# Optimization experiments

Measured on AMD Instinct MI355X. Metric: run time of the kernel, lower is better.

Reference implementation:

```python
import jax, jax.numpy as jnp
import numpy as np
from jax import lax

B = 32  # CS block size


def _conv(x, w, stride=1, pad=0):
    return lax.conv_general_dilated(
        x, w, window_strides=(stride, stride),
        padding=[(pad, pad), (pad, pad)],
        dimension_numbers=("NCHW", "OIHW", "NCHW"))


def _prelu(x, a):
    return jnp.where(x >= 0, x, a * x)


def _reshape_concat(x):
    # x: [N, B*B, h, w]; channel c = j*B + i maps to block pixel (i, j)
    # (tmp.view(B,B).permute(1,0) in the torch code). Blocks tile rows by
    # dim2 (h) and cols by dim3 (w). Vectorized depth-to-space + transpose.
    N, C, h, w = x.shape
    x5 = x.reshape(N, B, B, h, w)            # dims: (N, j, i, h, w)
    x5 = jnp.transpose(x5, (0, 3, 2, 4, 1))  # (N, h, i, w, j)
    return x5.reshape(N, 1, h * B, w * B)


def setup_inputs() -> dict:
    key = jax.random.key(0)
    ks = jax.random.split(key, 6)
    N, H, W = 16, 256, 256
    csnb = int(0.25 * B * B)  # 256
    inp = {
        "x": jax.random.normal(ks[0], (N, 1, H, W), jnp.float32),
        "W_cs": jax.random.normal(ks[1], (csnb, 1, B, B), jnp.float32) * 0.03,
        "W_init": jax.random.normal(ks[2], (B * B, csnb, 1, 1), jnp.float32) * 0.06,
        "W_first": jax.random.normal(ks[3], (64, 1, 3, 3), jnp.float32) * 0.3,
        "W_blk": jax.random.normal(ks[4], (64, 64, 3, 3), jnp.float32) * 0.04,
        "W_last": jax.random.normal(ks[5], (1, 64, 3, 3), jnp.float32) * 0.04,
        "a_main": jnp.full((1,), 0.1, jnp.float32),
        "a_blk": jnp.full((1,), 0.1, jnp.float32),
    }
    return inp


def reference(x, W_cs, W_init, W_first, W_blk, W_last, a_main, a_blk):
    # CS sampling: [N,1,H,W] -> [N,csnb,H/B,W/B]
    outcsy = _conv(x, W_cs, stride=B, pad=0)
    # initial reconstruction: 1x1 conv to B*B channels
    out = _conv(outcsy, W_init, stride=1, pad=0)
    out_initrec = _reshape_concat(out)          # [N,1,H,W]
    out = _prelu(_conv(out_initrec, W_first, pad=1), a_main)
    # same SORTRes_block (shared weights) applied 4 times
    for _ in range(4):
        o1 = _conv(out, W_blk, pad=1)
        o2 = _prelu(o1, a_blk)
        o3 = _conv(o2, W_blk, pad=1)
        out = _prelu(out + o3, a_blk)
    out = _conv(out + out_initrec, W_last, pad=1)
    return (out, outcsy, out_initrec)
```

## Files before the change

kernel.cpp:

```cpp
#include <hip/hip_runtime.h>
#include <hip/hip_bf16.h>
#include <initializer_list>


#define HW 65536
#define IMG 4194304

typedef __attribute__((ext_vector_type(8))) short short8;
typedef __attribute__((ext_vector_type(4))) float f32x4;

__device__ __forceinline__ float bf2f(unsigned short u) {
    union { unsigned u; float f; } v; v.u = ((unsigned)u) << 16; return v.f;
}
__device__ __forceinline__ unsigned short f2bf(float f) {
    union { float f; unsigned u; } v; v.f = f;
    unsigned r = v.u + 0x7FFF + ((v.u >> 16) & 1);
    return (unsigned short)(r >> 16);
}

__global__ void k_wcsT(const float* __restrict__ Wcs, float* __restrict__ WT)
{
    int e = blockIdx.x * 256 + threadIdx.x;
    int k = e >> 8, c = e & 255;
    WT[(long)k * 256 + c] = Wcs[(long)c * 1024 + k];
}

__global__ void k_winitT(const float* __restrict__ Wi, float* __restrict__ WT)
{
    int e = blockIdx.x * 256 + threadIdx.x;
    int ci = e >> 10, cc = e & 1023;
    WT[e] = Wi[(long)cc * 256 + ci];
}

__global__ __launch_bounds__(256) void k_cs2(const float* __restrict__ x,
        const float* __restrict__ WT, float* __restrict__ outcsy)
{
    __shared__ float xs[2][1024];
    const int b = blockIdx.x;
    const int tid = threadIdx.x;
#pragma unroll
    for (int t = 0; t < 2; ++t) {
        int p = b * 2 + t;
        int wb = p & 7, hb = (p >> 3) & 7, n = p >> 6;
#pragma unroll
        for (int i = 0; i < 4; ++i) {
            int k = tid + 256 * i;
            int ii = k >> 5, jj = k & 31;
            xs[t][k] = x[(long)n * HW + (hb * 32 + ii) * 256 + wb * 32 + jj];
        }
    }
    __syncthreads();
    float a0 = 0.f, a1 = 0.f;
    for (int k = 0; k < 1024; k += 8) {
#pragma unroll
        for (int u = 0; u < 8; ++u) {
            float wv = WT[(long)(k + u) * 256 + tid];
            a0 += wv * xs[0][k + u];
            a1 += wv * xs[1][k + u];
        }
    }
#pragma unroll
    for (int t = 0; t < 2; ++t) {
        int p = b * 2 + t;
        int wb = p & 7, hb = (p >> 3) & 7, n = p >> 6;
        float a = t ? a1 : a0;
        outcsy[(long)n * 16384 + tid * 64 + hb * 8 + wb] = a;
    }
}

__global__ __launch_bounds__(256) void k_init2(const float* __restrict__ outcsy,
        const float* __restrict__ WT, float* __restrict__ initrec)
{
    __shared__ float ys[2][256];
    __shared__ float ov[2][1024];
    const int b = blockIdx.x;
    const int np = b & 7, s = b >> 3;
    const int wb = s & 7, hb = s >> 3;
    const int tid = threadIdx.x;
#pragma unroll
    for (int i = 0; i < 2; ++i) {
        int idx = tid + 256 * i;
        int t = idx >> 8, c = idx & 255;
        ys[t][c] = outcsy[(long)(np * 2 + t) * 16384 + c * 64 + s];
    }
    __syncthreads();
#pragma unroll
    for (int q4 = 0; q4 < 4; ++q4) {
        int cc = q4 * 256 + tid;
        float a0 = 0.f, a1 = 0.f;
        for (int ci = 0; ci < 256; ci += 8) {
#pragma unroll
            for (int u = 0; u < 8; ++u) {
                float wv = WT[(long)(ci + u) * 1024 + cc];
                a0 += wv * ys[0][ci + u];
                a1 += wv * ys[1][ci + u];
            }
        }
        int i = cc & 31, j = cc >> 5;
        ov[0][i * 32 + j] = a0;
        ov[1][i * 32 + j] = a1;
    }
    __syncthreads();
#pragma unroll
    for (int t = 0; t < 2; ++t) {
        int n = np * 2 + t;
#pragma unroll
        for (int i2 = 0; i2 < 4; ++i2) {
            int p = i2 * 256 + tid;
            int i = p >> 5, j = p & 31;
            initrec[(long)n * HW + (hb * 32 + i) * 256 + wb * 32 + j] = ov[t][p];
        }
    }
}

__global__ __launch_bounds__(256) void k_first(const float* __restrict__ initrec,
        const float* __restrict__ Wf, unsigned short* __restrict__ A,
        const float* __restrict__ alpha_p)
{
    const int bid = blockIdx.x;
    const int tx = bid & 15, ty = (bid >> 4) & 15, n = bid >> 8;
    const int tid = threadIdx.x;
    const int x = (tx << 4) + (tid & 15), y = (ty << 4) + (tid >> 4);
    const float* ip = initrec + (long)n * HW;

    float in[9];
#pragma unroll
    for (int ky = 0; ky < 3; ++ky)
#pragma unroll
        for (int kx = 0; kx < 3; ++kx) {
            int iy = y + ky - 1, ix = x + kx - 1;
            in[ky * 3 + kx] = ((unsigned)iy < 256u && (unsigned)ix < 256u)
                                  ? ip[iy * 256 + ix] : 0.f;
        }

    const float alpha = alpha_p[0];
    unsigned short* op = &A[(((long)n * 256 + y) * 256 + x) * 64];
#pragma unroll
    for (int c8 = 0; c8 < 8; ++c8) {
        short8 ov;
#pragma unroll
        for (int j = 0; j < 8; ++j) {
            const float* wp = &Wf[(c8 * 8 + j) * 9];
            float a = 0.f;
#pragma unroll
            for (int t = 0; t < 9; ++t) a += wp[t] * in[t];
            a = a >= 0.f ? a : alpha * a;
            ov[j] = (short)f2bf(a);
        }
        *(short8*)&op[c8 * 8] = ov;
    }
}

__global__ void k_wprep(const float* __restrict__ Wb, unsigned short* __restrict__ Wp)
{
    int e = blockIdx.x * 256 + threadIdx.x;
    int cc = e / 18432, r = e % 18432;
    int tap = r / 2048, r2 = r % 2048;
    int nt = (r2 >> 9) & 3, l = (r2 >> 3) & 63, j = r2 & 7;
    int co = nt * 16 + (l & 15);
    int ci = cc * 32 + (l >> 4) * 8 + j;
    Wp[e] = f2bf(Wb[co * 576 + ci * 9 + tap]);
}

__global__ __launch_bounds__(256, 2) void k_res(const unsigned short* __restrict__ src,
        unsigned short* __restrict__ dst, const unsigned short* __restrict__ Wp,
        const float* __restrict__ alpha_p)
{
    __shared__ short smem[30400];

    const int tid = threadIdx.x;
    const int bid = blockIdx.x;
    const int tx = bid & 15, ty = (bid >> 4) & 15, n = bid >> 8;
    const int x0 = tx * 16, y0 = ty * 16;
    const int w = tid >> 6, lane = tid & 63;
    const int q = lane >> 4, mm = lane & 15;
    const float alpha = alpha_p[0];
    const unsigned short* sb = src + (long)n * IMG;

    int pb1[6];
#pragma unroll
    for (int i = 0; i < 6; ++i) {
        int p = (w + 4 * i) * 16 + mm;
        p = p < 323 ? p : 323;
        pb1[i] = p + 2 * (p / 18);
    }

#pragma unroll
    for (int i = 0; i < 13; ++i) {
        int idx = tid + 256 * i;
        if (idx < 3200) {
            int pix = idx >> 3, part = idx & 7;
            int row = pix / 20, col = pix - row * 20;
            int gy = y0 + row - 2, gx = x0 + col - 2;
            short8 v = {0, 0, 0, 0, 0, 0, 0, 0};
            if ((unsigned)gy < 256u && (unsigned)gx < 256u)
                v = *(const short8*)&sb[((long)gy * 256 + gx) * 64 + part * 8];
            *(short8*)&smem[pix * 76 + part * 8] = v;
        }
    }

    short8 bcur[4], bnxt[4];
#pragma unroll
    for (int nt = 0; nt < 4; ++nt)
        bcur[nt] = *(const short8*)&Wp[(size_t)(nt * 512 + lane * 8)];

    const f32x4 zz = {0.f, 0.f, 0.f, 0.f};
    f32x4 acc1[6][4];
#pragma unroll
    for (int i = 0; i < 6; ++i)
#pragma unroll
        for (int nt = 0; nt < 4; ++nt) acc1[i][nt] = zz;

    __syncthreads();

#pragma unroll
    for (int s = 0; s < 18; ++s) {
        const int cc = s / 9, tap = s % 9;
        int un = s + 1; un = un < 18 ? un : 0;
#pragma unroll
        for (int nt = 0; nt < 4; ++nt)
            bnxt[nt] = *(const short8*)&Wp[(size_t)(un / 9) * 18432 +
                       (size_t)(((un % 9) * 4 + nt) * 512 + lane * 8)];
        const int ky = tap / 3, kx = tap % 3;
        const int toff = (ky * 20 + kx) * 76 + cc * 32 + q * 8;
#pragma unroll
        for (int i = 0; i < 5; ++i) {
            short8 af = *(const short8*)&smem[pb1[i] * 76 + toff];
#pragma unroll
            for (int nt = 0; nt < 4; ++nt)
                acc1[i][nt] = __builtin_amdgcn_mfma_f32_16x16x32_bf16(
                    af, bcur[nt], acc1[i][nt], 0, 0, 0);
        }
        if (w == 0) {
            short8 af = *(const short8*)&smem[pb1[5] * 76 + toff];
#pragma unroll
            for (int nt = 0; nt < 4; ++nt)
                acc1[5][nt] = __builtin_amdgcn_mfma_f32_16x16x32_bf16(
                    af, bcur[nt], acc1[5][nt], 0, 0, 0);
        }
#pragma unroll
        for (int nt = 0; nt < 4; ++nt) bcur[nt] = bnxt[nt];
    }
    __syncthreads();

#pragma unroll
    for (int i = 0; i < 6; ++i) {
        int t = w + 4 * i;
        if (t < 21) {
#pragma unroll
            for (int r = 0; r < 4; ++r) {
                int p = t * 16 + q * 4 + r;
                p = p < 323 ? p : 323;
                int rho = p / 18, gam = p - 18 * rho;
                bool valid = (unsigned)(y0 - 1 + rho) < 256u &&
                             (unsigned)(x0 - 1 + gam) < 256u;
#pragma unroll
                for (int nt = 0; nt < 4; ++nt) {
                    float v = acc1[i][nt][r];
                    v = v >= 0.f ? v : alpha * v;
                    smem[p * 76 + nt * 16 + mm] = valid ? (short)f2bf(v) : (short)0;
                }
            }
        }
    }
    __syncthreads();

    f32x4 acc2[4][4];
#pragma unroll
    for (int mt = 0; mt < 4; ++mt)
#pragma unroll
        for (int nt = 0; nt < 4; ++nt) acc2[mt][nt] = zz;

#pragma unroll
    for (int s = 0; s < 18; ++s) {
        const int cc = s / 9, tap = s % 9;
        int un = s + 1; un = un < 18 ? un : 17;
#pragma unroll
        for (int nt = 0; nt < 4; ++nt)
            bnxt[nt] = *(const short8*)&Wp[(size_t)(un / 9) * 18432 +
                       (size_t)(((un % 9) * 4 + nt) * 512 + lane * 8)];
        const int ky = tap / 3, kx = tap % 3;
#pragma unroll
        for (int mt = 0; mt < 4; ++mt) {
            int pix = (4 * w + mt + ky) * 18 + mm + kx;
            short8 af = *(const short8*)&smem[pix * 76 + cc * 32 + q * 8];
#pragma unroll
            for (int nt = 0; nt < 4; ++nt)
                acc2[mt][nt] = __builtin_amdgcn_mfma_f32_16x16x32_bf16(
                    af, bcur[nt], acc2[mt][nt], 0, 0, 0);
        }
#pragma unroll
        for (int nt = 0; nt < 4; ++nt) bcur[nt] = bnxt[nt];
    }
    __syncthreads();

    unsigned short* ob = (unsigned short*)smem;
#pragma unroll
    for (int mt = 0; mt < 4; ++mt) {
        int row = 4 * w + mt;
#pragma unroll
        for (int nt = 0; nt < 4; ++nt)
#pragma unroll
            for (int r = 0; r < 4; ++r) {
                int xx = q * 4 + r;
                ob[(row * 16 + xx) * 64 + nt * 16 + mm] = f2bf(acc2[mt][nt][r]);
            }
    }
    __syncthreads();
#pragma unroll
    for (int i = 0; i < 8; ++i) {
        int e = (tid + 256 * i) * 8;
        int co = e & 63, xx = (e >> 6) & 15, row = e >> 10;
        long g = (((long)n * 256 + y0 + row) * 256 + (x0 + xx)) * 64 + co;
        short8 cv = *(short8*)&ob[e];
        short8 rv = *(const short8*)&src[(long)n * IMG +
                                         ((long)(y0 + row) * 256 + x0 + xx) * 64 + co];
        short8 ov;
#pragma unroll
        for (int j = 0; j < 8; ++j) {
            float v = bf2f((unsigned short)cv[j]) + bf2f((unsigned short)rv[j]);
            v = (v >= 0.f) ? v : alpha * v;
            ov[j] = (short)f2bf(v);
        }
        *(short8*)&dst[(long)n * IMG + ((long)(y0 + row) * 256 + x0 + xx) * 64 + co] = ov;
    }
}

__global__ __launch_bounds__(256) void k_last(const unsigned short* __restrict__ A,
        const float* __restrict__ initrec, const float* __restrict__ Wl,
        float* __restrict__ out0)
{
    __shared__ short ibuf[23328];
    const int bid = blockIdx.x;
    const int tx = bid & 15, ty = (bid >> 4) & 15, n = bid >> 8;
    const int x0 = tx * 16, y0 = ty * 16;
    const int tid = threadIdx.x;
    const unsigned short* Ab = A + (long)n * IMG;

#pragma unroll
    for (int i = 0; i < 11; ++i) {
        int idx = tid + 256 * i;
        if (idx < 2592) {
            int pix = idx >> 3, part = idx & 7;
            int row = pix / 18, col = pix - row * 18;
            int gy = y0 + row - 1, gx = x0 + col - 1;
            short8 v = {0, 0, 0, 0, 0, 0, 0, 0};
            if ((unsigned)gy < 256u && (unsigned)gx < 256u)
                v = *(const short8*)&Ab[((long)gy * 256 + gx) * 64 + part * 8];
            *(short8*)&ibuf[pix * 72 + part * 8] = v;
        }
    }
    __syncthreads();

    float wsum[9];
#pragma unroll
    for (int k = 0; k < 9; ++k) wsum[k] = 0.f;
    for (int ci = 0; ci < 64; ++ci)
#pragma unroll
        for (int k = 0; k < 9; ++k) wsum[k] += Wl[ci * 9 + k];

    const int x = tid & 15, y = tid >> 4;
    const float* ip = initrec + (long)n * HW;
    float acc = 0.f;
#pragma unroll
    for (int ky = 0; ky < 3; ++ky) {
#pragma unroll
        for (int kx = 0; kx < 3; ++kx) {
            const int tap = ky * 3 + kx;
            const short* p = &ibuf[((y + ky) * 18 + (x + kx)) * 72];
#pragma unroll
            for (int c8 = 0; c8 < 8; ++c8) {
                short8 av = *(const short8*)&p[c8 * 8];
#pragma unroll
                for (int j = 0; j < 8; ++j)
                    acc += Wl[(c8 * 8 + j) * 9 + tap] * bf2f((unsigned short)av[j]);
            }
            int gy = y0 + y + ky - 1, gx = x0 + x + kx - 1;
            if ((unsigned)gy < 256u && (unsigned)gx < 256u)
                acc += wsum[tap] * ip[gy * 256 + gx];
        }
    }
    out0[((long)n * 256 + y0 + y) * 256 + (x0 + x)] = acc;
}

extern "C" void kernel_launch(void* const* d_in, const int* in_sizes, int n_in,
                              void* d_out, int out_size, void* d_ws, size_t ws_size,
                              hipStream_t stream)
{
    const float* x     = (const float*)d_in[0];
    const float* Wcs   = (const float*)d_in[1];
    const float* Winit = (const float*)d_in[2];
    const float* Wf    = (const float*)d_in[3];
    const float* Wb    = (const float*)d_in[4];
    const float* Wl    = (const float*)d_in[5];
    const float* amain = (const float*)d_in[6];
    const float* ablk  = (const float*)d_in[7];

    float* out0    = (float*)d_out;
    float* outcsy  = out0 + 1048576;
    float* initrec = outcsy + 262144;

    const size_t EXTRA = 73728 + 2 * 1048576;
    unsigned short* A = (unsigned short*)d_ws;
    int nc = 1;
    for (int c : {16, 8, 4, 2, 1})
        if ((size_t)(16 + c) * IMG * 2 + EXTRA <= ws_size) { nc = c; break; }
    unsigned short* Bt   = A + (size_t)16 * IMG;
    unsigned short* Wp   = Bt + (size_t)nc * IMG;
    float*          WcsT = (float*)(Wp + 36864);
    float*          WinT = WcsT + 262144;

    k_wcsT<<<1024, 256, 0, stream>>>(Wcs, WcsT);
    k_winitT<<<1024, 256, 0, stream>>>(Winit, WinT);
    k_wprep<<<144, 256, 0, stream>>>(Wb, Wp);

    k_cs2<<<512, 256, 0, stream>>>(x, WcsT, outcsy);
    k_init2<<<512, 256, 0, stream>>>(outcsy, WinT, initrec);
    k_first<<<4096, 256, 0, stream>>>(initrec, Wf, A, amain);

    for (int n0 = 0; n0 < 16; n0 += nc) {
        unsigned short* Ac = A + (size_t)n0 * IMG;
        for (int i = 0; i < 4; ++i) {
            const unsigned short* s = (i & 1) ? Bt : Ac;
            unsigned short*       d = (i & 1) ? Ac : Bt;
            k_res<<<nc * 256, 256, 0, stream>>>(s, d, Wp, ablk);
        }
    }
    k_last<<<4096, 256, 0, stream>>>(A, initrec, Wl, out0);
}
```

Measured before the change: 1.141 ms.

## Split residual-block halo load by channel half and swizzle output staging

The residual-block kernel now loads only the first 32 input channels of the halo tile into shared memory before the first conv starts. The second channel half is prefetched into registers and stored to shared memory after the first nine taps, so its global latency overlaps MFMA work. The output staging buffer also gets an XOR swizzle across 8-element channel groups to cut LDS bank conflicts on the scalar bf16 writes. The cost is extra registers for the prefetch (seven short8 values plus offsets), which may lower occupancy, and an added barrier.

After: 1.095 ms (median of 2 runs). -4.0%, faster.

```diff
diff --git a/kernel.cpp b/kernel.cpp
--- a/kernel.cpp
+++ b/kernel.cpp
@@ -186,10 +186,10 @@
     }
 
 #pragma unroll
-    for (int i = 0; i < 13; ++i) {
+    for (int i = 0; i < 7; ++i) {
         int idx = tid + 256 * i;
-        if (idx < 3200) {
-            int pix = idx >> 3, part = idx & 7;
+        if (idx < 1600) {
+            int pix = idx >> 2, part = idx & 3;
             int row = pix / 20, col = pix - row * 20;
             int gy = y0 + row - 2, gx = x0 + col - 2;
             short8 v = {0, 0, 0, 0, 0, 0, 0, 0};
@@ -199,6 +199,23 @@
         }
     }
 
+    short8 pre[7];
+    int pofs[7];
+#pragma unroll
+    for (int i = 0; i < 7; ++i) {
+        short8 z = {0, 0, 0, 0, 0, 0, 0, 0};
+        pre[i] = z; pofs[i] = -1;
+        int idx = tid + 256 * i;
+        if (idx < 1600) {
+            int pix = idx >> 2, part = (idx & 3) + 4;
+            int row = pix / 20, col = pix - row * 20;
+            int gy = y0 + row - 2, gx = x0 + col - 2;
+            pofs[i] = pix * 76 + part * 8;
+            if ((unsigned)gy < 256u && (unsigned)gx < 256u)
+                pre[i] = *(const short8*)&sb[((long)gy * 256 + gx) * 64 + part * 8];
+        }
+    }
+
     short8 bcur[4], bnxt[4];
 #pragma unroll
     for (int nt = 0; nt < 4; ++nt)
@@ -214,15 +231,49 @@
     __syncthreads();
 
 #pragma unroll
-    for (int s = 0; s < 18; ++s) {
-        const int cc = s / 9, tap = s % 9;
-        int un = s + 1; un = un < 18 ? un : 0;
+    for (int s = 0; s < 9; ++s) {
+        const int tap = s;
+        const int un = s + 1;
 #pragma unroll
         for (int nt = 0; nt < 4; ++nt)
             bnxt[nt] = *(const short8*)&Wp[(size_t)(un / 9) * 18432 +
                        (size_t)(((un % 9) * 4 + nt) * 512 + lane * 8)];
         const int ky = tap / 3, kx = tap % 3;
-        const int toff = (ky * 20 + kx) * 76 + cc * 32 + q * 8;
+        const int toff = (ky * 20 + kx) * 76 + q * 8;
+#pragma unroll
+        for (int i = 0; i < 5; ++i) {
+            short8 af = *(const short8*)&smem[pb1[i] * 76 + toff];
+#pragma unroll
+            for (int nt = 0; nt < 4; ++nt)
+                acc1[i][nt] = __builtin_amdgcn_mfma_f32_16x16x32_bf16(
+                    af, bcur[nt], acc1[i][nt], 0, 0, 0);
+        }
+        if (w == 0) {
+            short8 af = *(const short8*)&smem[pb1[5] * 76 + toff];
+#pragma unroll
+            for (int nt = 0; nt < 4; ++nt)
+                acc1[5][nt] = __builtin_amdgcn_mfma_f32_16x16x32_bf16(
+                    af, bcur[nt], acc1[5][nt], 0, 0, 0);
+        }
+#pragma unroll
+        for (int nt = 0; nt < 4; ++nt) bcur[nt] = bnxt[nt];
+    }
+
+#pragma unroll
+    for (int i = 0; i < 7; ++i)
+        if (pofs[i] >= 0) *(short8*)&smem[pofs[i]] = pre[i];
+    __syncthreads();
+
+#pragma unroll
+    for (int s = 9; s < 18; ++s) {
+        const int tap = s - 9;
+        int un = s + 1; un = un < 18 ? un : 0;
+#pragma unroll
+        for (int nt = 0; nt < 4; ++nt)
+            bnxt[nt] = *(const short8*)&Wp[(size_t)(un / 9) * 18432 +
+                       (size_t)(((un % 9) * 4 + nt) * 512 + lane * 8)];
+        const int ky = tap / 3, kx = tap % 3;
+        const int toff = (ky * 20 + kx) * 76 + 32 + q * 8;
 #pragma unroll
         for (int i = 0; i < 5; ++i) {
             short8 af = *(const short8*)&smem[pb1[i] * 76 + toff];
@@ -299,22 +350,28 @@
     for (int mt = 0; mt < 4; ++mt) {
         int row = 4 * w + mt;
 #pragma unroll
-        for (int nt = 0; nt < 4; ++nt)
-#pragma unroll
-            for (int r = 0; r < 4; ++r) {
-                int xx = q * 4 + r;
-                ob[(row * 16 + xx) * 64 + nt * 16 + mm] = f2bf(acc2[mt][nt][r]);
+        for (int r = 0; r < 4; ++r) {
+            int px = row * 16 + q * 4 + r;
+            int h = (px >> 2) & 7;
+#pragma unroll
+            for (int nt = 0; nt < 4; ++nt) {
+                int sg = nt * 2 + (mm >> 3);
+                int swz = ((sg ^ h) << 3) | (mm & 7);
+                ob[px * 64 + swz] = f2bf(acc2[mt][nt][r]);
             }
+        }
     }
     __syncthreads();
 #pragma unroll
     for (int i = 0; i < 8; ++i) {
-        int e = (tid + 256 * i) * 8;
-        int co = e & 63, xx = (e >> 6) & 15, row = e >> 10;
+        int c = tid + 256 * i;
+        int px = c >> 3, k = c & 7;
+        int row = px >> 4, xx = px & 15;
+        int h = (px >> 2) & 7;
+        int co = (k ^ h) << 3;
         long g = (((long)n * 256 + y0 + row) * 256 + (x0 + xx)) * 64 + co;
-        short8 cv = *(short8*)&ob[e];
-        short8 rv = *(const short8*)&src[(long)n * IMG +
-                                         ((long)(y0 + row) * 256 + x0 + xx) * 64 + co];
+        short8 cv = *(short8*)&ob[px * 64 + k * 8];
+        short8 rv = *(const short8*)&src[g];
         short8 ov;
 #pragma unroll
         for (int j = 0; j < 8; ++j) {
@@ -322,7 +379,7 @@
             v = (v >= 0.f) ? v : alpha * v;
             ov[j] = (short)f2bf(v);
         }
-        *(short8*)&dst[(long)n * IMG + ((long)(y0 + row) * 256 + x0 + xx) * 64 + co] = ov;
+        *(short8*)&dst[g] = ov;
     }
 }
 
```
